# Kernel tuning notes

Hardware: AMD Instinct MI355X
Metric: run time of the kernel (lower is better)

## Reference

```python
import jax, jax.numpy as jnp
import numpy as np

B, S, D, H = 4, 2048, 1024, 16
HD = D // H
OUT = 256

def setup_inputs() -> dict:
    key = jax.random.key(0)
    ks = jax.random.split(key, 11)
    s = 0.02
    return {
        'query': jax.random.normal(ks[0], (B, S, D), jnp.float32),
        'key':   jax.random.normal(ks[1], (B, S, D), jnp.float32),
        'value': jax.random.normal(ks[2], (B, S, D), jnp.float32),
        'Wq': jax.random.normal(ks[3], (D, D), jnp.float32) * s,
        'bq': jnp.zeros((D,), jnp.float32),
        'Wk': jax.random.normal(ks[4], (D, D), jnp.float32) * s,
        'bk': jnp.zeros((D,), jnp.float32),
        'Wv': jax.random.normal(ks[5], (D, D), jnp.float32) * s,
        'bv': jnp.zeros((D,), jnp.float32),
        'Wf': jax.random.normal(ks[6], (D, OUT), jnp.float32) * s,
        'bf': jnp.zeros((OUT,), jnp.float32),
    }

def softmax_1(x):
    # exp(x) / (1 + sum(exp(x)))  -- numerically as written in the source
    e = jnp.exp(x)
    return e / (1.0 + e.sum(axis=-1, keepdims=True))

def reference(query, key, value, Wq, bq, Wk, bk, Wv, bv, Wf, bf):
    scale = jnp.sqrt(jnp.asarray(HD, jnp.float32))
    def heads(x, W, b):
        return (x @ W + b).reshape(B, S, H, HD).transpose(0, 2, 1, 3)  # [B,H,S,HD]
    Q = heads(query, Wq, bq)
    K = heads(key, Wk, bk)
    V = heads(value, Wv, bv)
    energy = jnp.einsum('bhqd,bhkd->bhqk', Q, K) / scale  # [B,H,S,S]
    attn = softmax_1(energy)
    x = jnp.einsum('bhqk,bhkd->bhqd', attn, V)  # dropout is identity in eval
    x = x.transpose(0, 2, 1, 3).reshape(B, S, D)
    return x @ Wf + bf  # [B,S,256]
```

## Files before the change

kernel.cpp:

```cpp
#include <hip/hip_runtime.h>
#include <stdint.h>

#define DI __device__ __forceinline__

typedef __attribute__((ext_vector_type(8))) short bf16x8;
typedef __attribute__((ext_vector_type(4))) float f32x4;
typedef __attribute__((ext_vector_type(8))) unsigned short u16x8;
typedef __attribute__((ext_vector_type(2))) unsigned int u32x2;
typedef __attribute__((ext_vector_type(4))) unsigned int u32x4;

static constexpr int BATCH = 4, SEQ = 2048, DIM = 1024, NH = 16, HDIM = 64, DOUT = 256;
static constexpr int MROWS = BATCH * SEQ;

DI unsigned short f2b(float f) {
  union { float f; unsigned u; } v; v.f = f;
  unsigned u = v.u + 0x7FFFu + ((v.u >> 16) & 1u);
  return (unsigned short)(u >> 16);
}

DI float ex2(float x) {
#if __has_builtin(__builtin_amdgcn_exp2f)
  return __builtin_amdgcn_exp2f(x);
#else
  float r; asm("v_exp_f32 %0, %1" : "=v"(r) : "v"(x)); return r;
#endif
}

DI unsigned cvtpk(float lo, float hi) {
  unsigned r; asm("v_cvt_pk_bf16_f32 %0, %1, %2" : "=v"(r) : "v"(lo), "v"(hi)); return r;
}

typedef const __attribute__((address_space(1))) unsigned int* gp1;
typedef __attribute__((address_space(3))) unsigned int* lp3;
DI void gload16(const void* g, void* l) {
  __builtin_amdgcn_global_load_lds((gp1)g, (lp3)l, 16, 0, 0);
}

__global__ void k_tcvt3(const float* __restrict__ s0, const float* __restrict__ s1,
                        const float* __restrict__ s2, unsigned short* __restrict__ d, int R, int C) {
  __shared__ float t[32][33];
  const float* s = (blockIdx.z == 0) ? s0 : (blockIdx.z == 1) ? s1 : s2;
  unsigned short* dz = d + (size_t)blockIdx.z * R * C;
  int c0 = blockIdx.x * 32, r0 = blockIdx.y * 32;
  int tx = threadIdx.x, ty = threadIdx.y;
#pragma unroll
  for (int j = 0; j < 32; j += 8)
    t[ty + j][tx] = s[(size_t)(r0 + ty + j) * C + c0 + tx];
  __syncthreads();
#pragma unroll
  for (int j = 0; j < 32; j += 8)
    dz[(size_t)(c0 + ty + j) * R + r0 + tx] = f2b(t[tx][ty + j]);
}

__global__ void k_tcvt(const float* __restrict__ s, unsigned short* __restrict__ d, int R, int C) {
  __shared__ float t[32][33];
  int c0 = blockIdx.x * 32, r0 = blockIdx.y * 32;
  int tx = threadIdx.x, ty = threadIdx.y;
#pragma unroll
  for (int j = 0; j < 32; j += 8)
    t[ty + j][tx] = s[(size_t)(r0 + ty + j) * C + c0 + tx];
  __syncthreads();
#pragma unroll
  for (int j = 0; j < 32; j += 8)
    d[(size_t)(c0 + ty + j) * R + r0 + tx] = f2b(t[tx][ty + j]);
}

__global__ __launch_bounds__(256, 2) void k_gemm3(
    const float* __restrict__ Aq, const float* __restrict__ Ak, const float* __restrict__ Av,
    const unsigned short* __restrict__ Wt3,
    const float* __restrict__ bq, const float* __restrict__ bk, const float* __restrict__ bv,
    unsigned short* __restrict__ Qh, unsigned short* __restrict__ Kh,
    unsigned short* __restrict__ Vtb, float qscale) {
  __shared__ unsigned short Al[128 * 32];
  __shared__ unsigned short Bl[128 * 32];
  const int tid = threadIdx.x, wid = tid >> 6, lane = tid & 63;
  const int m0 = blockIdx.x * 128, n0 = blockIdx.y * 128;
  const int z = blockIdx.z;
  const int wr = wid >> 1, wc = wid & 1;
  const int g = lane >> 4, r16 = lane & 15;
  const int K = DIM;

  const float* Af = (z == 0) ? Aq : (z == 1) ? Ak : Av;
  const unsigned short* Bt = Wt3 + (size_t)z * DIM * DIM;
  const float* bias = (z == 0) ? bq : (z == 1) ? bk : bv;
  const float scale = (z == 0) ? qscale : 1.0f;

  const int ra = tid >> 2, ca = (tid & 3) * 8;
  const int rb = (256 + tid) >> 2, cb = ((256 + tid) & 3) * 8;
  float4 ar[2][2];
  {
    const float4* pa = reinterpret_cast<const float4*>(Af + (size_t)(m0 + ra) * K + ca);
    const float4* pb = reinterpret_cast<const float4*>(Af + (size_t)(m0 + rb) * K + cb);
    ar[0][0] = pa[0]; ar[0][1] = pa[1];
    ar[1][0] = pb[0]; ar[1][1] = pb[1];
  }

  f32x4 acc[4][4];
#pragma unroll
  for (int i = 0; i < 4; ++i)
#pragma unroll
    for (int j = 0; j < 4; ++j) acc[i][j] = f32x4{0.f, 0.f, 0.f, 0.f};

  for (int kk = 0; kk < K; kk += 32) {
    u32x4 w0{cvtpk(ar[0][0].x, ar[0][0].y), cvtpk(ar[0][0].z, ar[0][0].w),
             cvtpk(ar[0][1].x, ar[0][1].y), cvtpk(ar[0][1].z, ar[0][1].w)};
    *reinterpret_cast<u32x4*>(&Al[ra * 32 + ca]) = w0;
    u32x4 w1{cvtpk(ar[1][0].x, ar[1][0].y), cvtpk(ar[1][0].z, ar[1][0].w),
             cvtpk(ar[1][1].x, ar[1][1].y), cvtpk(ar[1][1].z, ar[1][1].w)};
    *reinterpret_cast<u32x4*>(&Al[rb * 32 + cb]) = w1;
#pragma unroll
    for (int is = 0; is < 2; ++is) {
      int slot = (is * 4 + wid) * 64 + lane;
      int row = slot >> 2, ch = slot & 3;
      gload16(Bt + (size_t)(n0 + row) * K + kk + ch * 8, &Bl[(is * 4 + wid) * 64 * 8]);
    }
    __syncthreads();
    if (kk + 32 < K) {
      const float4* pa = reinterpret_cast<const float4*>(Af + (size_t)(m0 + ra) * K + kk + 32 + ca);
      const float4* pb = reinterpret_cast<const float4*>(Af + (size_t)(m0 + rb) * K + kk + 32 + cb);
      ar[0][0] = pa[0]; ar[0][1] = pa[1];
      ar[1][0] = pb[0]; ar[1][1] = pb[1];
    }
    bf16x8 af[4], bfv[4];
#pragma unroll
    for (int i = 0; i < 4; ++i)
      af[i] = *reinterpret_cast<const bf16x8*>(&Al[(wr * 64 + i * 16 + r16) * 32 + g * 8]);
#pragma unroll
    for (int j = 0; j < 4; ++j)
      bfv[j] = *reinterpret_cast<const bf16x8*>(&Bl[(wc * 64 + j * 16 + r16) * 32 + g * 8]);
#pragma unroll
    for (int i = 0; i < 4; ++i)
#pragma unroll
      for (int j = 0; j < 4; ++j)
        acc[i][j] = __builtin_amdgcn_mfma_f32_16x16x32_bf16(af[i], bfv[j], acc[i][j], 0, 0, 0);
    __syncthreads();
  }

  const int rr = g * 4;
#pragma unroll
  for (int i = 0; i < 4; ++i) {
#pragma unroll
    for (int j = 0; j < 4; ++j) {
#pragma unroll
      for (int q = 0; q < 4; ++q) {
        int mrow = m0 + wr * 64 + i * 16 + rr + q;
        int ncol = n0 + wc * 64 + j * 16 + r16;
        float v = (acc[i][j][q] + bias[ncol]) * scale;
        int b_ = mrow >> 11, s_ = mrow & 2047;
        int h_ = ncol >> 6, hd = ncol & 63;
        if (z == 2) {
          Vtb[(((size_t)(b_ * NH + h_) * HDIM + hd) << 11) + s_] = f2b(v);
        } else {
          unsigned short* dst = (z == 0) ? Qh : Kh;
          dst[(((size_t)(b_ * NH + h_) * SEQ + s_) << 6) + hd] = f2b(v);
        }
      }
    }
  }
}

__global__ __launch_bounds__(256, 2) void k_gemmf(
    const unsigned short* __restrict__ A, const unsigned short* __restrict__ Bt,
    const float* __restrict__ bias, float* __restrict__ out, int K, int N) {
  __shared__ unsigned short Al[128 * 32];
  __shared__ unsigned short Bl[128 * 32];
  const int tid = threadIdx.x, wid = tid >> 6, lane = tid & 63;
  const int m0 = blockIdx.x * 128, n0 = blockIdx.y * 128;
  const int wr = wid >> 1, wc = wid & 1;
  const int g = lane >> 4, r16 = lane & 15;

  f32x4 acc[4][4];
#pragma unroll
  for (int i = 0; i < 4; ++i)
#pragma unroll
    for (int j = 0; j < 4; ++j) acc[i][j] = f32x4{0.f, 0.f, 0.f, 0.f};

  for (int kk = 0; kk < K; kk += 32) {
#pragma unroll
    for (int is = 0; is < 2; ++is) {
      int slot = (is * 4 + wid) * 64 + lane;
      int row = slot >> 2, ch = slot & 3;
      gload16(A + (size_t)(m0 + row) * K + kk + ch * 8, &Al[(is * 4 + wid) * 64 * 8]);
    }
#pragma unroll
    for (int is = 0; is < 2; ++is) {
      int slot = (is * 4 + wid) * 64 + lane;
      int row = slot >> 2, ch = slot & 3;
      gload16(Bt + (size_t)(n0 + row) * K + kk + ch * 8, &Bl[(is * 4 + wid) * 64 * 8]);
    }
    __syncthreads();
    bf16x8 af[4], bfv[4];
#pragma unroll
    for (int i = 0; i < 4; ++i)
      af[i] = *reinterpret_cast<const bf16x8*>(&Al[(wr * 64 + i * 16 + r16) * 32 + g * 8]);
#pragma unroll
    for (int j = 0; j < 4; ++j)
      bfv[j] = *reinterpret_cast<const bf16x8*>(&Bl[(wc * 64 + j * 16 + r16) * 32 + g * 8]);
#pragma unroll
    for (int i = 0; i < 4; ++i)
#pragma unroll
      for (int j = 0; j < 4; ++j)
        acc[i][j] = __builtin_amdgcn_mfma_f32_16x16x32_bf16(af[i], bfv[j], acc[i][j], 0, 0, 0);
    __syncthreads();
  }

  const int rr = g * 4;
#pragma unroll
  for (int i = 0; i < 4; ++i)
#pragma unroll
    for (int j = 0; j < 4; ++j)
#pragma unroll
      for (int q = 0; q < 4; ++q) {
        int mrow = m0 + wr * 64 + i * 16 + rr + q;
        int ncol = n0 + wc * 64 + j * 16 + r16;
        out[(size_t)mrow * N + ncol] = acc[i][j][q] + bias[ncol];
      }
}

__global__ __launch_bounds__(256, 4) void k_attn(
    const unsigned short* __restrict__ Qh, const unsigned short* __restrict__ Kh,
    const unsigned short* __restrict__ Vt, unsigned short* __restrict__ X) {
  __shared__ unsigned short Kl[64 * 64];
  __shared__ unsigned short Vl[64 * 64];
  __shared__ unsigned short Pl[128 * 64];

  const int tid = threadIdx.x, wid = tid >> 6, lane = tid & 63;
  const int g = lane >> 4, r16 = lane & 15;
  const int bh = blockIdx.y, b_ = bh >> 4, h_ = bh & 15;
  const int q0 = blockIdx.x * 128;
  const unsigned short* Qp = Qh + ((size_t)bh * SEQ + q0) * HDIM;
  const unsigned short* Kp = Kh + (size_t)bh * SEQ * HDIM;
  const unsigned short* Vp = Vt + (size_t)bh * HDIM * SEQ;
  const int qw = wid * 32;

  bf16x8 qf[2][2];
#pragma unroll
  for (int fr = 0; fr < 2; ++fr)
#pragma unroll
    for (int ks = 0; ks < 2; ++ks)
      qf[fr][ks] = *reinterpret_cast<const bf16x8*>(
          Qp + (size_t)(qw + fr * 16 + r16) * HDIM + ks * 32 + g * 8);

  bf16x8 vones;
#pragma unroll
  for (int i = 0; i < 8; ++i) vones[i] = (r16 == 0) ? (short)0x3F80 : (short)0;

  const int slot0 = wid * 64 + lane, slot1 = (4 + wid) * 64 + lane;
  const int sr0 = slot0 >> 3, sc0 = (slot0 & 7) ^ (sr0 & 7);
  const int sr1 = slot1 >> 3, sc1 = (slot1 & 7) ^ (sr1 & 7);
  const unsigned short* Ks0 = Kp + (size_t)sr0 * HDIM + sc0 * 8;
  const unsigned short* Ks1 = Kp + (size_t)sr1 * HDIM + sc1 * 8;
  const unsigned short* Vs0 = Vp + (size_t)sr0 * SEQ + sc0 * 8;
  const unsigned short* Vs1 = Vp + (size_t)sr1 * SEQ + sc1 * 8;
  const int ld0 = wid * 512, ld1 = (4 + wid) * 512;

  f32x4 o[2][4], ol[2];
#pragma unroll
  for (int fr = 0; fr < 2; ++fr) {
#pragma unroll
    for (int hf = 0; hf < 4; ++hf) o[fr][hf] = f32x4{0.f, 0.f, 0.f, 0.f};
    ol[fr] = f32x4{0.f, 0.f, 0.f, 0.f};
  }

  for (int t = 0; t < SEQ / 64; ++t) {
    __syncthreads();
    {
      const size_t koff = (size_t)t * 64 * HDIM;
      const int voff = t * 64;
      gload16(Ks0 + koff, &Kl[ld0]);
      gload16(Ks1 + koff, &Kl[ld1]);
      gload16(Vs0 + voff, &Vl[ld0]);
      gload16(Vs1 + voff, &Vl[ld1]);
    }
    __syncthreads();

    f32x4 s_[2][4];
#pragma unroll
    for (int fr = 0; fr < 2; ++fr)
#pragma unroll
      for (int cf = 0; cf < 4; ++cf) s_[fr][cf] = f32x4{0.f, 0.f, 0.f, 0.f};
#pragma unroll
    for (int cf = 0; cf < 4; ++cf) {
      int krow = cf * 16 + r16;
#pragma unroll
      for (int ks = 0; ks < 2; ++ks) {
        bf16x8 kf = *reinterpret_cast<const bf16x8*>(
            &Kl[krow * 64 + (((ks * 4 + g) ^ (krow & 7)) << 3)]);
#pragma unroll
        for (int fr = 0; fr < 2; ++fr)
          s_[fr][cf] = __builtin_amdgcn_mfma_f32_16x16x32_bf16(kf, qf[fr][ks], s_[fr][cf], 0, 0, 0);
      }
    }

#pragma unroll
    for (int fr = 0; fr < 2; ++fr) {
      int prow = qw + fr * 16 + r16;
      int base = prow * 64, swz = prow & 7;
#pragma unroll
      for (int cf = 0; cf < 4; ++cf) {
        float p0 = ex2(s_[fr][cf][0]);
        float p1 = ex2(s_[fr][cf][1]);
        float p2 = ex2(s_[fr][cf][2]);
        float p3 = ex2(s_[fr][cf][3]);
        unsigned w0 = cvtpk(p0, p1);
        unsigned w1 = cvtpk(p2, p3);
        int off = base + (((cf * 2 + (g >> 1)) ^ swz) << 3) + (g & 1) * 4;
        *reinterpret_cast<u32x2*>(&Pl[off]) = u32x2{w0, w1};
      }
    }
    __syncthreads();

#pragma unroll
    for (int ks = 0; ks < 2; ++ks) {
      bf16x8 pf[2];
#pragma unroll
      for (int fr = 0; fr < 2; ++fr) {
        int prow = qw + fr * 16 + r16;
        pf[fr] = *reinterpret_cast<const bf16x8*>(
            &Pl[prow * 64 + (((ks * 4 + g) ^ (prow & 7)) << 3)]);
      }
#pragma unroll
      for (int hf = 0; hf < 4; ++hf) {
        int vrow = hf * 16 + r16;
        bf16x8 vf = *reinterpret_cast<const bf16x8*>(
            &Vl[vrow * 64 + (((ks * 4 + g) ^ (vrow & 7)) << 3)]);
#pragma unroll
        for (int fr = 0; fr < 2; ++fr)
          o[fr][hf] = __builtin_amdgcn_mfma_f32_16x16x32_bf16(pf[fr], vf, o[fr][hf], 0, 0, 0);
      }
#pragma unroll
      for (int fr = 0; fr < 2; ++fr)
        ol[fr] = __builtin_amdgcn_mfma_f32_16x16x32_bf16(pf[fr], vones, ol[fr], 0, 0, 0);
    }
  }

#pragma unroll
  for (int fr = 0; fr < 2; ++fr) {
#pragma unroll
    for (int q = 0; q < 4; ++q) {
      float lsum = __shfl(ol[fr][q], lane & 48, 64);
      float inv = 1.0f / (1.0f + lsum);
      int row = q0 + qw + fr * 16 + g * 4 + q;
      unsigned short* xp = X + (size_t)(b_ * SEQ + row) * DIM + h_ * 64;
#pragma unroll
      for (int hf = 0; hf < 4; ++hf) xp[hf * 16 + r16] = f2b(o[fr][hf][q] * inv);
    }
  }
}

extern "C" void kernel_launch(void* const* d_in, const int* in_sizes, int n_in,
                              void* d_out, int out_size, void* d_ws, size_t ws_size,
                              hipStream_t stream) {
  const float* q  = (const float*)d_in[0];
  const float* k  = (const float*)d_in[1];
  const float* v  = (const float*)d_in[2];
  const float* Wq = (const float*)d_in[3];
  const float* bq = (const float*)d_in[4];
  const float* Wk = (const float*)d_in[5];
  const float* bk = (const float*)d_in[6];
  const float* Wv = (const float*)d_in[7];
  const float* bv = (const float*)d_in[8];
  const float* Wf = (const float*)d_in[9];
  const float* bf = (const float*)d_in[10];

  char* ws = (char*)d_ws;
  unsigned short* Abuf = (unsigned short*)ws;
  unsigned short* Wt3  = (unsigned short*)(ws + (size_t)16777216);
  unsigned short* Wtf  = Wt3 + (size_t)3 * DIM * DIM;
  unsigned short* Qh   = Wtf + (size_t)DOUT * DIM;
  unsigned short* Kh   = Qh + (size_t)MROWS * DIM;
  unsigned short* Vtb  = Kh + (size_t)MROWS * DIM;

  dim3 b256(256);
  dim3 tb(32, 8);

  const float qscale = 0.125f * 1.44269504088896f;

  k_tcvt3<<<dim3(32, 32, 3), tb, 0, stream>>>(Wq, Wk, Wv, Wt3, DIM, DIM);
  k_tcvt<<<dim3(8, 32), tb, 0, stream>>>(Wf, Wtf, DIM, DOUT);
  k_gemm3<<<dim3(64, 8, 3), b256, 0, stream>>>(q, k, v, Wt3, bq, bk, bv, Qh, Kh, Vtb, qscale);
  k_attn<<<dim3(16, 64), b256, 0, stream>>>(Qh, Kh, Vtb, Abuf);
  k_gemmf<<<dim3(64, 2), b256, 0, stream>>>(Abuf, Wtf, bf, (float*)d_out, DIM, DOUT);
}
```

Before: 189.9 us.

## Double K-tile depth in QKV projection GEMM and add XOR-swizzled LDS layout

The fused QKV projection GEMM now processes a K-step of 64 instead of 32 per iteration, which halves the number of barrier pairs and loop iterations. Each thread prefetches 8 float4 of A per step. The LDS tiles for A and B are XOR-swizzled by row so the wider 64-element rows do not cause bank conflicts on the MFMA fragment reads. The cost is double the LDS and more prefetch registers, which may reduce occupancy below the two blocks per SM requested by the launch bounds.

```diff
diff --git a/kernel.cpp b/kernel.cpp
--- a/kernel.cpp
+++ b/kernel.cpp
@@ -71,8 +71,8 @@
     const float* __restrict__ bq, const float* __restrict__ bk, const float* __restrict__ bv,
     unsigned short* __restrict__ Qh, unsigned short* __restrict__ Kh,
     unsigned short* __restrict__ Vtb, float qscale) {
-  __shared__ unsigned short Al[128 * 32];
-  __shared__ unsigned short Bl[128 * 32];
+  __shared__ unsigned short Al[128 * 64];
+  __shared__ unsigned short Bl[128 * 64];
   const int tid = threadIdx.x, wid = tid >> 6, lane = tid & 63;
   const int m0 = blockIdx.x * 128, n0 = blockIdx.y * 128;
   const int z = blockIdx.z;
@@ -85,14 +85,13 @@
   const float* bias = (z == 0) ? bq : (z == 1) ? bk : bv;
   const float scale = (z == 0) ? qscale : 1.0f;
 
-  const int ra = tid >> 2, ca = (tid & 3) * 8;
-  const int rb = (256 + tid) >> 2, cb = ((256 + tid) & 3) * 8;
-  float4 ar[2][2];
+  const int ra = tid >> 1, ha = (tid & 1) * 32;
+  const int ha8 = (tid & 1) * 4, rsw = ra & 7;
+  float4 ar[8];
   {
-    const float4* pa = reinterpret_cast<const float4*>(Af + (size_t)(m0 + ra) * K + ca);
-    const float4* pb = reinterpret_cast<const float4*>(Af + (size_t)(m0 + rb) * K + cb);
-    ar[0][0] = pa[0]; ar[0][1] = pa[1];
-    ar[1][0] = pb[0]; ar[1][1] = pb[1];
+    const float4* pa = reinterpret_cast<const float4*>(Af + (size_t)(m0 + ra) * K + ha);
+#pragma unroll
+    for (int j = 0; j < 8; ++j) ar[j] = pa[j];
   }
 
   f32x4 acc[4][4];
@@ -101,38 +100,45 @@
 #pragma unroll
     for (int j = 0; j < 4; ++j) acc[i][j] = f32x4{0.f, 0.f, 0.f, 0.f};
 
-  for (int kk = 0; kk < K; kk += 32) {
-    u32x4 w0{cvtpk(ar[0][0].x, ar[0][0].y), cvtpk(ar[0][0].z, ar[0][0].w),
-             cvtpk(ar[0][1].x, ar[0][1].y), cvtpk(ar[0][1].z, ar[0][1].w)};
-    *reinterpret_cast<u32x4*>(&Al[ra * 32 + ca]) = w0;
-    u32x4 w1{cvtpk(ar[1][0].x, ar[1][0].y), cvtpk(ar[1][0].z, ar[1][0].w),
-             cvtpk(ar[1][1].x, ar[1][1].y), cvtpk(ar[1][1].z, ar[1][1].w)};
-    *reinterpret_cast<u32x4*>(&Al[rb * 32 + cb]) = w1;
-#pragma unroll
-    for (int is = 0; is < 2; ++is) {
+  for (int kk = 0; kk < K; kk += 64) {
+#pragma unroll
+    for (int j2 = 0; j2 < 4; ++j2) {
+      u32x4 w{cvtpk(ar[2 * j2].x, ar[2 * j2].y), cvtpk(ar[2 * j2].z, ar[2 * j2].w),
+              cvtpk(ar[2 * j2 + 1].x, ar[2 * j2 + 1].y), cvtpk(ar[2 * j2 + 1].z, ar[2 * j2 + 1].w)};
+      *reinterpret_cast<u32x4*>(&Al[ra * 64 + (((ha8 + j2) ^ rsw) << 3)]) = w;
+    }
+#pragma unroll
+    for (int is = 0; is < 4; ++is) {
       int slot = (is * 4 + wid) * 64 + lane;
-      int row = slot >> 2, ch = slot & 3;
-      gload16(Bt + (size_t)(n0 + row) * K + kk + ch * 8, &Bl[(is * 4 + wid) * 64 * 8]);
-    }
-    __syncthreads();
-    if (kk + 32 < K) {
-      const float4* pa = reinterpret_cast<const float4*>(Af + (size_t)(m0 + ra) * K + kk + 32 + ca);
-      const float4* pb = reinterpret_cast<const float4*>(Af + (size_t)(m0 + rb) * K + kk + 32 + cb);
-      ar[0][0] = pa[0]; ar[0][1] = pa[1];
-      ar[1][0] = pb[0]; ar[1][1] = pb[1];
-    }
-    bf16x8 af[4], bfv[4];
-#pragma unroll
-    for (int i = 0; i < 4; ++i)
-      af[i] = *reinterpret_cast<const bf16x8*>(&Al[(wr * 64 + i * 16 + r16) * 32 + g * 8]);
-#pragma unroll
-    for (int j = 0; j < 4; ++j)
-      bfv[j] = *reinterpret_cast<const bf16x8*>(&Bl[(wc * 64 + j * 16 + r16) * 32 + g * 8]);
-#pragma unroll
-    for (int i = 0; i < 4; ++i)
-#pragma unroll
-      for (int j = 0; j < 4; ++j)
-        acc[i][j] = __builtin_amdgcn_mfma_f32_16x16x32_bf16(af[i], bfv[j], acc[i][j], 0, 0, 0);
+      int row = slot >> 3, ch = slot & 7;
+      int sch = ch ^ (row & 7);
+      gload16(Bt + (size_t)(n0 + row) * K + kk + sch * 8, &Bl[(is * 4 + wid) * 512]);
+    }
+    __syncthreads();
+    if (kk + 64 < K) {
+      const float4* pa = reinterpret_cast<const float4*>(Af + (size_t)(m0 + ra) * K + kk + 64 + ha);
+#pragma unroll
+      for (int j = 0; j < 8; ++j) ar[j] = pa[j];
+    }
+#pragma unroll
+    for (int ks = 0; ks < 2; ++ks) {
+      bf16x8 af[4], bfv[4];
+#pragma unroll
+      for (int i = 0; i < 4; ++i) {
+        int row = wr * 64 + i * 16 + r16;
+        af[i] = *reinterpret_cast<const bf16x8*>(&Al[row * 64 + (((ks * 4 + g) ^ (row & 7)) << 3)]);
+      }
+#pragma unroll
+      for (int j = 0; j < 4; ++j) {
+        int row = wc * 64 + j * 16 + r16;
+        bfv[j] = *reinterpret_cast<const bf16x8*>(&Bl[row * 64 + (((ks * 4 + g) ^ (row & 7)) << 3)]);
+      }
+#pragma unroll
+      for (int i = 0; i < 4; ++i)
+#pragma unroll
+        for (int j = 0; j < 4; ++j)
+          acc[i][j] = __builtin_amdgcn_mfma_f32_16x16x32_bf16(af[i], bfv[j], acc[i][j], 0, 0, 0);
+    }
     __syncthreads();
   }
 
```

Measured after the change: 228.6 us. 20.4% more time.
